# Kernel tuning notes

Measured on AMD Instinct MI355X. Metric: run time of the kernel, lower is better.

Reference implementation:

```python
import jax, jax.numpy as jnp
import numpy as np
from jax import lax

SINKHORN_ITERS = 20


def sinkhorn_knopp(logits, tau=1.0, iterations=SINKHORN_ITERS):
    # logits: [N, K]. Log-domain alternating row/col normalization.
    N, K = logits.shape
    P = logits / tau
    log_target_col_sum = jnp.log(jnp.asarray(N / K, dtype=logits.dtype) + 1e-9)

    def step(P, _):
        P = P - jax.nn.logsumexp(P, axis=1, keepdims=True)   # row sums -> 1
        P = P - jax.nn.logsumexp(P, axis=0, keepdims=True) + log_target_col_sum  # col sums -> N/K
        return P, None

    P, _ = lax.scan(step, P, None, length=iterations)
    return jnp.exp(P)


def setup_inputs() -> dict:
    key = jax.random.key(0)
    ks = jax.random.split(key, 8)
    N, C, K, B = 200000, 128, 32, 16
    x = jax.random.normal(ks[0], (N, C), dtype=jnp.float32)
    batch = jnp.sort(jax.random.randint(ks[1], (N,), 0, B))
    # assign_mlp: Linear(C,C) -> ReLU -> Linear(C,K)
    W1 = jax.random.normal(ks[2], (C, C), dtype=jnp.float32) / np.sqrt(C)
    b1 = jnp.zeros((C,), dtype=jnp.float32)
    W2 = jax.random.normal(ks[3], (C, K), dtype=jnp.float32) / np.sqrt(C)
    b2 = jnp.zeros((K,), dtype=jnp.float32)
    scaling = jnp.asarray(5.0, dtype=jnp.float32)
    return {"x": x, "batch": batch, "W1": W1, "b1": b1, "W2": W2, "b2": b2,
            "scaling": scaling, "num_graphs": B}


def reference(x, batch, W1, b1, W2, b2, scaling, num_graphs):
    # assignment logits: MLP(x) * scaling  -> [N, K]
    h = jax.nn.relu(x @ W1 + b1)
    logits = (h @ W2 + b2) * scaling
    # doubly-stochastic soft assignment via Sinkhorn-Knopp (tau=1.0, 20 iters)
    s = sinkhorn_knopp(logits, tau=1.0, iterations=SINKHORN_ITERS)  # [N, K]
    # pooled super-node features: scatter-sum over graphs of s[n,k]*x[n,c]
    onehot = jax.nn.one_hot(batch, num_graphs, dtype=x.dtype)        # [N, B]
    out = jnp.einsum('nb,nk,nc->bkc', onehot, s, x)                  # [B, K, C]
    return out
```

## Files before the change

### kernel.cpp

```cpp
#include <hip/hip_runtime.h>
#include <hip/hip_bf16.h>

#define C_DIM 128
#define K_DIM 32
#define N_ITERS 20
#define SPAD 132
#define NSHARD 8

__global__ void init_kernel(float* __restrict__ out, float* __restrict__ vcs,
                            int n_out, int n_vcs) {
    int i = blockIdx.x * blockDim.x + threadIdx.x;
    int stride = gridDim.x * blockDim.x;
    for (int j = i; j < n_out; j += stride) out[j] = 0.f;
    for (int j = i; j < n_vcs; j += stride) vcs[j] = 0.f;
}

__global__ __launch_bounds__(1024, 4) void mlp_kernel(
    const float* __restrict__ x, const float* __restrict__ W1,
    const float* __restrict__ b1, const float* __restrict__ W2,
    const float* __restrict__ b2, const float* __restrict__ scal,
    float* __restrict__ Lg, int N, int ntiles) {
    __shared__ float sW1[C_DIM * C_DIM];
    __shared__ float sW2[C_DIM * K_DIM];
    __shared__ float sB1[C_DIM];
    __shared__ float sB2[K_DIM];
    __shared__ float sT[128][SPAD];

    const int tid = threadIdx.x;
    for (int i = tid; i < C_DIM * C_DIM / 4; i += 1024)
        ((float4*)sW1)[i] = ((const float4*)W1)[i];
    for (int i = tid; i < C_DIM * K_DIM / 4; i += 1024)
        ((float4*)sW2)[i] = ((const float4*)W2)[i];
    if (tid < C_DIM / 4) ((float4*)sB1)[tid] = ((const float4*)b1)[tid];
    if (tid < K_DIM / 4) ((float4*)sB2)[tid] = ((const float4*)b2)[tid];
    const float sc = *scal;

    const int wave = tid >> 6;
    const int lane = tid & 63;
    const int r0 = wave * 8;

    for (int tile = blockIdx.x; tile < ntiles; tile += gridDim.x) {
        const int row0 = tile * 128;
        const int rows = min(128, N - row0);
        __syncthreads();
        {
            const float4* src = (const float4*)(x + (size_t)row0 * C_DIM);
            for (int i = tid; i < rows * 32; i += 1024) {
                const int r = i >> 5, cq = i & 31;
                ((float4*)&sT[r][0])[cq] = src[i];
            }
        }
        __syncthreads();

        float acc[8][2];
#pragma unroll
        for (int r = 0; r < 8; ++r) {
            acc[r][0] = sB1[2 * lane];
            acc[r][1] = sB1[2 * lane + 1];
        }
#pragma unroll 2
        for (int kc = 0; kc < 32; ++kc) {
            const int k = kc * 4;
            const float2 w0 = *(const float2*)&sW1[(k + 0) * C_DIM + 2 * lane];
            const float2 w1 = *(const float2*)&sW1[(k + 1) * C_DIM + 2 * lane];
            const float2 w2 = *(const float2*)&sW1[(k + 2) * C_DIM + 2 * lane];
            const float2 w3 = *(const float2*)&sW1[(k + 3) * C_DIM + 2 * lane];
#pragma unroll
            for (int r = 0; r < 8; ++r) {
                const float4 xv = *(const float4*)&sT[r0 + r][k];
                acc[r][0] = fmaf(xv.x, w0.x, acc[r][0]);
                acc[r][1] = fmaf(xv.x, w0.y, acc[r][1]);
                acc[r][0] = fmaf(xv.y, w1.x, acc[r][0]);
                acc[r][1] = fmaf(xv.y, w1.y, acc[r][1]);
                acc[r][0] = fmaf(xv.z, w2.x, acc[r][0]);
                acc[r][1] = fmaf(xv.z, w2.y, acc[r][1]);
                acc[r][0] = fmaf(xv.w, w3.x, acc[r][0]);
                acc[r][1] = fmaf(xv.w, w3.y, acc[r][1]);
            }
        }
#pragma unroll
        for (int r = 0; r < 8; ++r) {
            float2 hv;
            hv.x = fmaxf(acc[r][0], 0.f);
            hv.y = fmaxf(acc[r][1], 0.f);
            *(float2*)&sT[r0 + r][2 * lane] = hv;
        }

        const int r2 = lane & 7;
        const int kk0 = (lane >> 3) * 4;
        float a2[4];
        a2[0] = sB2[kk0];
        a2[1] = sB2[kk0 + 1];
        a2[2] = sB2[kk0 + 2];
        a2[3] = sB2[kk0 + 3];
#pragma unroll 4
        for (int c = 0; c < C_DIM; c += 4) {
            const float4 hv = *(const float4*)&sT[r0 + r2][c];
            const float4 q0 = *(const float4*)&sW2[(c + 0) * K_DIM + kk0];
            const float4 q1 = *(const float4*)&sW2[(c + 1) * K_DIM + kk0];
            const float4 q2 = *(const float4*)&sW2[(c + 2) * K_DIM + kk0];
            const float4 q3 = *(const float4*)&sW2[(c + 3) * K_DIM + kk0];
            a2[0] = fmaf(hv.x, q0.x, a2[0]); a2[1] = fmaf(hv.x, q0.y, a2[1]);
            a2[2] = fmaf(hv.x, q0.z, a2[2]); a2[3] = fmaf(hv.x, q0.w, a2[3]);
            a2[0] = fmaf(hv.y, q1.x, a2[0]); a2[1] = fmaf(hv.y, q1.y, a2[1]);
            a2[2] = fmaf(hv.y, q1.z, a2[2]); a2[3] = fmaf(hv.y, q1.w, a2[3]);
            a2[0] = fmaf(hv.z, q2.x, a2[0]); a2[1] = fmaf(hv.z, q2.y, a2[1]);
            a2[2] = fmaf(hv.z, q2.z, a2[2]); a2[3] = fmaf(hv.z, q2.w, a2[3]);
            a2[0] = fmaf(hv.w, q3.x, a2[0]); a2[1] = fmaf(hv.w, q3.y, a2[1]);
            a2[2] = fmaf(hv.w, q3.z, a2[2]); a2[3] = fmaf(hv.w, q3.w, a2[3]);
        }
        const int g = row0 + r0 + r2;
        if (g < N) {
            float4 o = make_float4(a2[0] * sc, a2[1] * sc, a2[2] * sc, a2[3] * sc);
            *(float4*)&Lg[(size_t)g * K_DIM + kk0] = o;
        }
    }
}

__device__ __forceinline__ int bitrev5(int l) {
    return ((l & 1) << 4) | ((l & 2) << 2) | (l & 4) | ((l & 8) >> 2) |
           ((l & 16) >> 4);
}

#define FOLD_STAGE(M, HALF)                                   \
    {                                                         \
        const bool hi = (lane & (M)) != 0;                    \
        _Pragma("unroll")                                     \
        for (int j = 0; j < (HALF); ++j) {                    \
            const float give = hi ? p[j] : p[j + (HALF)];     \
            const float keep = hi ? p[j + (HALF)] : p[j];     \
            p[j] = keep + __shfl_xor(give, (M));              \
        }                                                     \
    }

__global__ __launch_bounds__(1024) void sinkhorn_iter_kernel(
    const float* __restrict__ Lg, float* __restrict__ vbuf,
    float* __restrict__ shards, int t, int N) {
    __shared__ float sv[K_DIM];
    __shared__ float swsum[16][K_DIM];
    const int tid = threadIdx.x;
    const int wave = tid >> 6;
    const int lane = tid & 63;

    if (tid < K_DIM) {
        float vp = 0.f;
        if (t > 1) {
            float cs = 0.f;
#pragma unroll
            for (int sh = 0; sh < NSHARD; ++sh)
                cs += shards[((size_t)(t - 1) * NSHARD + sh) * K_DIM + tid];
            vp = vbuf[(t - 2) * K_DIM + tid] + __logf(cs) -
                 __logf((float)N / (float)K_DIM);
        }
        sv[tid] = vp;
        if (blockIdx.x == 0) vbuf[(t - 1) * K_DIM + tid] = vp;
    }
    __syncthreads();

    const size_t n = (size_t)blockIdx.x * 1024 + tid;
    float p[K_DIM];
    if (n < (size_t)N) {
        const float4* Lr = (const float4*)(Lg + n * K_DIM);
#pragma unroll
        for (int j = 0; j < 8; ++j) {
            const float4 lv = Lr[j];
            p[4 * j + 0] = lv.x - sv[4 * j + 0];
            p[4 * j + 1] = lv.y - sv[4 * j + 1];
            p[4 * j + 2] = lv.z - sv[4 * j + 2];
            p[4 * j + 3] = lv.w - sv[4 * j + 3];
        }
        float m0 = p[0];
#pragma unroll
        for (int j = 1; j < K_DIM; ++j) m0 = fmaxf(m0, p[j]);
        float sum = 0.f;
#pragma unroll
        for (int j = 0; j < K_DIM; ++j) {
            p[j] = __expf(p[j] - m0);
            sum += p[j];
        }
        const float inv = 1.f / sum;
#pragma unroll
        for (int j = 0; j < K_DIM; ++j) p[j] *= inv;
    } else {
#pragma unroll
        for (int j = 0; j < K_DIM; ++j) p[j] = 0.f;
    }

    FOLD_STAGE(1, 16)
    FOLD_STAGE(2, 8)
    FOLD_STAGE(4, 4)
    FOLD_STAGE(8, 2)
    FOLD_STAGE(16, 1)
    const float tot = p[0] + __shfl_xor(p[0], 32);
    if (lane < K_DIM) swsum[wave][bitrev5(lane)] = tot;
    __syncthreads();
    if (tid < K_DIM) {
        float s_ = 0.f;
#pragma unroll
        for (int w = 0; w < 16; ++w) s_ += swsum[w][tid];
        atomicAdd(&shards[((size_t)t * NSHARD + (blockIdx.x & (NSHARD - 1))) *
                              K_DIM + tid], s_);
    }
}

#define PCHUNK 96
#define PCH_PER_BLOCK 4

__global__ __launch_bounds__(256) void pool_kernel(
    const float* __restrict__ x, const int* __restrict__ batch,
    const float* __restrict__ Lg, const float* __restrict__ vbuf,
    const float* __restrict__ shards, float* __restrict__ out, int N) {
    __shared__ float sx[PCHUNK][C_DIM];
    __shared__ float ss[PCHUNK][K_DIM];
    __shared__ int sb[PCHUNK];
    __shared__ float sv19[K_DIM];
    __shared__ float sd[K_DIM];

    const int tid = threadIdx.x;
    if (tid < K_DIM) {
        sv19[tid] = vbuf[(N_ITERS - 1) * K_DIM + tid];
        float cs = 0.f;
#pragma unroll
        for (int sh = 0; sh < NSHARD; ++sh)
            cs += shards[((size_t)N_ITERS * NSHARD + sh) * K_DIM + tid];
        sd[tid] = ((float)N / (float)K_DIM) / cs;
    }
    __syncthreads();

    const int k0 = (tid >> 5) * 4;
    const int c0 = (tid & 31) * 4;
    float acc[4][4];
#pragma unroll
    for (int i = 0; i < 4; ++i)
#pragma unroll
        for (int j = 0; j < 4; ++j) acc[i][j] = 0.f;

    int cur_b = -1;
    const int base0 = blockIdx.x * (PCHUNK * PCH_PER_BLOCK);

    for (int cc = 0; cc < PCH_PER_BLOCK; ++cc) {
        const int base = base0 + cc * PCHUNK;
        if (base >= N) break;
        const int rows = min(PCHUNK, N - base);
        __syncthreads();
        {
            const float4* src = (const float4*)(x + (size_t)base * C_DIM);
            for (int i = tid; i < rows * (C_DIM / 4); i += 256)
                ((float4*)&sx[0][0])[i] = src[i];
        }
        if (tid < rows) {
            sb[tid] = batch[base + tid];
            const int n = base + tid;
            const float4* Lr = (const float4*)(Lg + (size_t)n * K_DIM);
            float p[K_DIM];
#pragma unroll
            for (int j = 0; j < 8; ++j) {
                const float4 lv = Lr[j];
                p[4 * j + 0] = lv.x - sv19[4 * j + 0];
                p[4 * j + 1] = lv.y - sv19[4 * j + 1];
                p[4 * j + 2] = lv.z - sv19[4 * j + 2];
                p[4 * j + 3] = lv.w - sv19[4 * j + 3];
            }
            float m0 = p[0];
#pragma unroll
            for (int j = 1; j < K_DIM; ++j) m0 = fmaxf(m0, p[j]);
            float sum = 0.f;
#pragma unroll
            for (int j = 0; j < K_DIM; ++j) {
                p[j] = __expf(p[j] - m0);
                sum += p[j];
            }
            const float inv = 1.f / sum;
#pragma unroll
            for (int j = 0; j < K_DIM; ++j) ss[tid][j] = p[j] * inv * sd[j];
        }
        __syncthreads();

        for (int r = 0; r < rows; ++r) {
            const int b = sb[r];
            if (b != cur_b) {
                if (cur_b >= 0) {
                    float* ob = out + ((size_t)cur_b * K_DIM + k0) * C_DIM + c0;
#pragma unroll
                    for (int i = 0; i < 4; ++i)
#pragma unroll
                        for (int j = 0; j < 4; ++j) {
                            atomicAdd(&ob[i * C_DIM + j], acc[i][j]);
                            acc[i][j] = 0.f;
                        }
                }
                cur_b = b;
            }
            const float4 sv = *(const float4*)&ss[r][k0];
            const float4 xv = *(const float4*)&sx[r][c0];
            const float sA[4] = {sv.x, sv.y, sv.z, sv.w};
            const float xA[4] = {xv.x, xv.y, xv.z, xv.w};
#pragma unroll
            for (int i = 0; i < 4; ++i)
#pragma unroll
                for (int j = 0; j < 4; ++j)
                    acc[i][j] = fmaf(sA[i], xA[j], acc[i][j]);
        }
    }
    if (cur_b >= 0) {
        float* ob = out + ((size_t)cur_b * K_DIM + k0) * C_DIM + c0;
#pragma unroll
        for (int i = 0; i < 4; ++i)
#pragma unroll
            for (int j = 0; j < 4; ++j) atomicAdd(&ob[i * C_DIM + j], acc[i][j]);
    }
}

extern "C" void kernel_launch(void* const* d_in, const int* in_sizes, int n_in,
                              void* d_out, int out_size, void* d_ws, size_t ws_size,
                              hipStream_t stream) {
    const float* x = (const float*)d_in[0];
    const int* batch = (const int*)d_in[1];
    const float* W1 = (const float*)d_in[2];
    const float* b1 = (const float*)d_in[3];
    const float* W2 = (const float*)d_in[4];
    const float* b2 = (const float*)d_in[5];
    const float* scal = (const float*)d_in[6];
    float* out = (float*)d_out;

    const int N = in_sizes[1];

    float* Lg = (float*)d_ws;
    float* vbuf = Lg + (size_t)N * K_DIM;
    float* shards = vbuf + (N_ITERS + 1) * K_DIM;
    const int n_vcs = (N_ITERS + 1) * K_DIM + (N_ITERS + 1) * NSHARD * K_DIM;

    init_kernel<<<64, 256, 0, stream>>>(out, vbuf, out_size, n_vcs);

    const int ntiles = (N + 127) / 128;
    mlp_kernel<<<256, 1024, 0, stream>>>(x, W1, b1, W2, b2, scal, Lg, N, ntiles);

    const int iblocks = (N + 1023) / 1024;
    for (int t = 1; t <= N_ITERS; ++t)
        sinkhorn_iter_kernel<<<iblocks, 1024, 0, stream>>>(Lg, vbuf, shards, t, N);

    const int pblocks = (N + PCHUNK * PCH_PER_BLOCK - 1) / (PCHUNK * PCH_PER_BLOCK);
    pool_kernel<<<pblocks, 256, 0, stream>>>(x, batch, Lg, vbuf, shards, out, N);
}
```

Baseline: 561.1 us.

## Use bf16 MFMA for MLP and fuse Sinkhorn iterations into persistent kernel

The MLP now converts x and the weights to bf16 and runs both layers on MFMA 16x16x32 instructions instead of scalar FP32 FMAs. The twenty per-iteration Sinkhorn launches are replaced by one kernel that keeps each row's logits in registers and uses a global arrival counter as a grid barrier between iterations. That kernel writes the final assignment matrix, so the pool kernel no longer recomputes the softmax. The grid barrier needs all 196 blocks of 1024 threads resident at once or it deadlocks, and bf16 inputs reduce logit precision.

New measurement: 1.422 ms. +153.5%, slower.

```diff
diff --git a/kernel.cpp b/kernel.cpp
--- a/kernel.cpp
+++ b/kernel.cpp
@@ -4,115 +4,117 @@
 #define C_DIM 128
 #define K_DIM 32
 #define N_ITERS 20
-#define SPAD 132
-#define NSHARD 8
-
-__global__ void init_kernel(float* __restrict__ out, float* __restrict__ vcs,
-                            int n_out, int n_vcs) {
+#define NSHARD 16
+#define WPAD 136
+
+typedef __attribute__((ext_vector_type(8))) short short8;
+typedef __attribute__((ext_vector_type(4))) float f32x4;
+typedef __attribute__((ext_vector_type(4))) unsigned short us4;
+
+__device__ __forceinline__ unsigned short f2bf(float f) {
+    __hip_bfloat16 h = __float2bfloat16(f);
+    return *reinterpret_cast<unsigned short*>(&h);
+}
+
+__global__ void init_kernel(float* __restrict__ out, int n_out,
+                            float* __restrict__ zreg, int n_z,
+                            const float* __restrict__ W1, const float* __restrict__ W2,
+                            unsigned short* __restrict__ W1t,
+                            unsigned short* __restrict__ W2t) {
     int i = blockIdx.x * blockDim.x + threadIdx.x;
     int stride = gridDim.x * blockDim.x;
     for (int j = i; j < n_out; j += stride) out[j] = 0.f;
-    for (int j = i; j < n_vcs; j += stride) vcs[j] = 0.f;
-}
-
-__global__ __launch_bounds__(1024, 4) void mlp_kernel(
-    const float* __restrict__ x, const float* __restrict__ W1,
-    const float* __restrict__ b1, const float* __restrict__ W2,
+    for (int j = i; j < n_z; j += stride) zreg[j] = 0.f;
+    for (int j = i; j < C_DIM * C_DIM; j += stride) {
+        int n = j >> 7, k = j & 127;
+        W1t[j] = f2bf(W1[k * C_DIM + n]);
+    }
+    for (int j = i; j < C_DIM * K_DIM; j += stride) {
+        int n = j >> 7, k = j & 127;
+        W2t[j] = f2bf(W2[k * K_DIM + n]);
+    }
+}
+
+__global__ __launch_bounds__(256, 4) void mlp_kernel(
+    const float* __restrict__ x, const unsigned short* __restrict__ W1t,
+    const float* __restrict__ b1, const unsigned short* __restrict__ W2t,
     const float* __restrict__ b2, const float* __restrict__ scal,
     float* __restrict__ Lg, int N, int ntiles) {
-    __shared__ float sW1[C_DIM * C_DIM];
-    __shared__ float sW2[C_DIM * K_DIM];
+    __shared__ unsigned short sW1[C_DIM][WPAD];
+    __shared__ unsigned short sW2[K_DIM][WPAD];
+    __shared__ unsigned short sX[64][WPAD];
+    __shared__ unsigned short sH[4][16][WPAD];
     __shared__ float sB1[C_DIM];
     __shared__ float sB2[K_DIM];
-    __shared__ float sT[128][SPAD];
 
     const int tid = threadIdx.x;
-    for (int i = tid; i < C_DIM * C_DIM / 4; i += 1024)
-        ((float4*)sW1)[i] = ((const float4*)W1)[i];
-    for (int i = tid; i < C_DIM * K_DIM / 4; i += 1024)
-        ((float4*)sW2)[i] = ((const float4*)W2)[i];
-    if (tid < C_DIM / 4) ((float4*)sB1)[tid] = ((const float4*)b1)[tid];
-    if (tid < K_DIM / 4) ((float4*)sB2)[tid] = ((const float4*)b2)[tid];
+    for (int i = tid; i < C_DIM * 16; i += 256) {
+        const int r = i >> 4, c8 = (i & 15) * 8;
+        *(float4*)&sW1[r][c8] = *(const float4*)&W1t[r * C_DIM + c8];
+    }
+    for (int i = tid; i < K_DIM * 16; i += 256) {
+        const int r = i >> 4, c8 = (i & 15) * 8;
+        *(float4*)&sW2[r][c8] = *(const float4*)&W2t[r * C_DIM + c8];
+    }
+    if (tid < C_DIM) sB1[tid] = b1[tid];
+    if (tid < K_DIM) sB2[tid] = b2[tid];
     const float sc = *scal;
 
     const int wave = tid >> 6;
     const int lane = tid & 63;
-    const int r0 = wave * 8;
+    const int lr = lane & 15;
+    const int kg = lane >> 4;
+    __syncthreads();
 
     for (int tile = blockIdx.x; tile < ntiles; tile += gridDim.x) {
-        const int row0 = tile * 128;
-        const int rows = min(128, N - row0);
-        __syncthreads();
-        {
-            const float4* src = (const float4*)(x + (size_t)row0 * C_DIM);
-            for (int i = tid; i < rows * 32; i += 1024) {
-                const int r = i >> 5, cq = i & 31;
-                ((float4*)&sT[r][0])[cq] = src[i];
-            }
-        }
-        __syncthreads();
-
-        float acc[8][2];
-#pragma unroll
-        for (int r = 0; r < 8; ++r) {
-            acc[r][0] = sB1[2 * lane];
-            acc[r][1] = sB1[2 * lane + 1];
-        }
-#pragma unroll 2
-        for (int kc = 0; kc < 32; ++kc) {
-            const int k = kc * 4;
-            const float2 w0 = *(const float2*)&sW1[(k + 0) * C_DIM + 2 * lane];
-            const float2 w1 = *(const float2*)&sW1[(k + 1) * C_DIM + 2 * lane];
-            const float2 w2 = *(const float2*)&sW1[(k + 2) * C_DIM + 2 * lane];
-            const float2 w3 = *(const float2*)&sW1[(k + 3) * C_DIM + 2 * lane];
-#pragma unroll
-            for (int r = 0; r < 8; ++r) {
-                const float4 xv = *(const float4*)&sT[r0 + r][k];
-                acc[r][0] = fmaf(xv.x, w0.x, acc[r][0]);
-                acc[r][1] = fmaf(xv.x, w0.y, acc[r][1]);
-                acc[r][0] = fmaf(xv.y, w1.x, acc[r][0]);
-                acc[r][1] = fmaf(xv.y, w1.y, acc[r][1]);
-                acc[r][0] = fmaf(xv.z, w2.x, acc[r][0]);
-                acc[r][1] = fmaf(xv.z, w2.y, acc[r][1]);
-                acc[r][0] = fmaf(xv.w, w3.x, acc[r][0]);
-                acc[r][1] = fmaf(xv.w, w3.y, acc[r][1]);
-            }
-        }
-#pragma unroll
-        for (int r = 0; r < 8; ++r) {
-            float2 hv;
-            hv.x = fmaxf(acc[r][0], 0.f);
-            hv.y = fmaxf(acc[r][1], 0.f);
-            *(float2*)&sT[r0 + r][2 * lane] = hv;
-        }
-
-        const int r2 = lane & 7;
-        const int kk0 = (lane >> 3) * 4;
-        float a2[4];
-        a2[0] = sB2[kk0];
-        a2[1] = sB2[kk0 + 1];
-        a2[2] = sB2[kk0 + 2];
-        a2[3] = sB2[kk0 + 3];
-#pragma unroll 4
-        for (int c = 0; c < C_DIM; c += 4) {
-            const float4 hv = *(const float4*)&sT[r0 + r2][c];
-            const float4 q0 = *(const float4*)&sW2[(c + 0) * K_DIM + kk0];
-            const float4 q1 = *(const float4*)&sW2[(c + 1) * K_DIM + kk0];
-            const float4 q2 = *(const float4*)&sW2[(c + 2) * K_DIM + kk0];
-            const float4 q3 = *(const float4*)&sW2[(c + 3) * K_DIM + kk0];
-            a2[0] = fmaf(hv.x, q0.x, a2[0]); a2[1] = fmaf(hv.x, q0.y, a2[1]);
-            a2[2] = fmaf(hv.x, q0.z, a2[2]); a2[3] = fmaf(hv.x, q0.w, a2[3]);
-            a2[0] = fmaf(hv.y, q1.x, a2[0]); a2[1] = fmaf(hv.y, q1.y, a2[1]);
-            a2[2] = fmaf(hv.y, q1.z, a2[2]); a2[3] = fmaf(hv.y, q1.w, a2[3]);
-            a2[0] = fmaf(hv.z, q2.x, a2[0]); a2[1] = fmaf(hv.z, q2.y, a2[1]);
-            a2[2] = fmaf(hv.z, q2.z, a2[2]); a2[3] = fmaf(hv.z, q2.w, a2[3]);
-            a2[0] = fmaf(hv.w, q3.x, a2[0]); a2[1] = fmaf(hv.w, q3.y, a2[1]);
-            a2[2] = fmaf(hv.w, q3.z, a2[2]); a2[3] = fmaf(hv.w, q3.w, a2[3]);
-        }
-        const int g = row0 + r0 + r2;
-        if (g < N) {
-            float4 o = make_float4(a2[0] * sc, a2[1] * sc, a2[2] * sc, a2[3] * sc);
-            *(float4*)&Lg[(size_t)g * K_DIM + kk0] = o;
+        const int row0 = tile * 64;
+        __syncthreads();
+        for (int i = tid; i < 2048; i += 256) {
+            const int r = i >> 5, c4 = (i & 31) * 4;
+            const float4 v = *(const float4*)&x[(size_t)(row0 + r) * C_DIM + c4];
+            us4 u;
+            u.x = f2bf(v.x); u.y = f2bf(v.y); u.z = f2bf(v.z); u.w = f2bf(v.w);
+            *(us4*)&sX[r][c4] = u;
+        }
+        __syncthreads();
+
+        short8 a[4];
+#pragma unroll
+        for (int kt = 0; kt < 4; ++kt)
+            a[kt] = *(const short8*)&sX[wave * 16 + lr][kt * 32 + kg * 8];
+#pragma unroll
+        for (int ct = 0; ct < 8; ++ct) {
+            const float bv = sB1[ct * 16 + lr];
+            f32x4 acc = {bv, bv, bv, bv};
+#pragma unroll
+            for (int kt = 0; kt < 4; ++kt) {
+                const short8 b = *(const short8*)&sW1[ct * 16 + lr][kt * 32 + kg * 8];
+                acc = __builtin_amdgcn_mfma_f32_16x16x32_bf16(a[kt], b, acc, 0, 0, 0);
+            }
+#pragma unroll
+            for (int r = 0; r < 4; ++r)
+                sH[wave][kg * 4 + r][ct * 16 + lr] = f2bf(fmaxf(acc[r], 0.f));
+        }
+        __syncthreads();
+
+        short8 a2[4];
+#pragma unroll
+        for (int kt = 0; kt < 4; ++kt)
+            a2[kt] = *(const short8*)&sH[wave][lr][kt * 32 + kg * 8];
+#pragma unroll
+        for (int ct = 0; ct < 2; ++ct) {
+            const float bv = sB2[ct * 16 + lr];
+            f32x4 acc = {bv, bv, bv, bv};
+#pragma unroll
+            for (int kt = 0; kt < 4; ++kt) {
+                const short8 b = *(const short8*)&sW2[ct * 16 + lr][kt * 32 + kg * 8];
+                acc = __builtin_amdgcn_mfma_f32_16x16x32_bf16(a2[kt], b, acc, 0, 0, 0);
+            }
+#pragma unroll
+            for (int r = 0; r < 4; ++r) {
+                const int g = row0 + wave * 16 + kg * 4 + r;
+                Lg[(size_t)g * K_DIM + ct * 16 + lr] = acc[r] * sc;
+            }
         }
     }
 }
@@ -133,73 +135,110 @@
         }                                                     \
     }
 
-__global__ __launch_bounds__(1024) void sinkhorn_iter_kernel(
-    const float* __restrict__ Lg, float* __restrict__ vbuf,
-    float* __restrict__ shards, int t, int N) {
+__global__ __launch_bounds__(1024, 4) void sinkhorn_kernel(
+    float* __restrict__ Lg, float* __restrict__ shards, int* __restrict__ arrive,
+    int N, int nblocks) {
     __shared__ float sv[K_DIM];
     __shared__ float swsum[16][K_DIM];
+    __shared__ float sdl[K_DIM];
     const int tid = threadIdx.x;
     const int wave = tid >> 6;
     const int lane = tid & 63;
-
-    if (tid < K_DIM) {
-        float vp = 0.f;
-        if (t > 1) {
+    const size_t n = (size_t)blockIdx.x * 1024 + tid;
+    const bool valid = n < (size_t)N;
+    const int myshard = blockIdx.x & (NSHARD - 1);
+    const float log_tgt = __logf((float)N / (float)K_DIM);
+
+    if (tid < K_DIM) sv[tid] = 0.f;
+
+    float L[K_DIM];
+    if (valid) {
+        const float4* Lr = (const float4*)(Lg + n * K_DIM);
+#pragma unroll
+        for (int j = 0; j < 8; ++j) {
+            const float4 v = Lr[j];
+            L[4 * j] = v.x; L[4 * j + 1] = v.y; L[4 * j + 2] = v.z; L[4 * j + 3] = v.w;
+        }
+    } else {
+#pragma unroll
+        for (int j = 0; j < K_DIM; ++j) L[j] = 0.f;
+    }
+    __syncthreads();
+
+    float m0 = 0.f, inv = 0.f;
+    for (int t = 1; t <= N_ITERS; ++t) {
+        float p[K_DIM];
+        if (valid) {
+#pragma unroll
+            for (int j = 0; j < K_DIM; ++j) p[j] = L[j] - sv[j];
+            m0 = p[0];
+#pragma unroll
+            for (int j = 1; j < K_DIM; ++j) m0 = fmaxf(m0, p[j]);
+            float sum = 0.f;
+#pragma unroll
+            for (int j = 0; j < K_DIM; ++j) {
+                p[j] = __expf(p[j] - m0);
+                sum += p[j];
+            }
+            inv = 1.f / sum;
+#pragma unroll
+            for (int j = 0; j < K_DIM; ++j) p[j] *= inv;
+        } else {
+#pragma unroll
+            for (int j = 0; j < K_DIM; ++j) p[j] = 0.f;
+        }
+
+        FOLD_STAGE(1, 16)
+        FOLD_STAGE(2, 8)
+        FOLD_STAGE(4, 4)
+        FOLD_STAGE(8, 2)
+        FOLD_STAGE(16, 1)
+        const float tot = p[0] + __shfl_xor(p[0], 32);
+        if (lane < K_DIM) swsum[wave][bitrev5(lane)] = tot;
+        __syncthreads();
+        if (tid < K_DIM) {
+            float s_ = 0.f;
+#pragma unroll
+            for (int w = 0; w < 16; ++w) s_ += swsum[w][tid];
+            atomicAdd(&shards[((size_t)t * NSHARD + myshard) * K_DIM + tid], s_);
+        }
+        __syncthreads();
+        __threadfence();
+        if (tid == 0) {
+            __hip_atomic_fetch_add(arrive + t, 1, __ATOMIC_RELEASE,
+                                   __HIP_MEMORY_SCOPE_AGENT);
+            while (__hip_atomic_load(arrive + t, __ATOMIC_ACQUIRE,
+                                     __HIP_MEMORY_SCOPE_AGENT) < nblocks)
+                __builtin_amdgcn_s_sleep(2);
+        }
+        __syncthreads();
+
+        if (tid < K_DIM) {
             float cs = 0.f;
 #pragma unroll
             for (int sh = 0; sh < NSHARD; ++sh)
-                cs += shards[((size_t)(t - 1) * NSHARD + sh) * K_DIM + tid];
-            vp = vbuf[(t - 2) * K_DIM + tid] + __logf(cs) -
-                 __logf((float)N / (float)K_DIM);
-        }
-        sv[tid] = vp;
-        if (blockIdx.x == 0) vbuf[(t - 1) * K_DIM + tid] = vp;
-    }
-    __syncthreads();
-
-    const size_t n = (size_t)blockIdx.x * 1024 + tid;
-    float p[K_DIM];
-    if (n < (size_t)N) {
-        const float4* Lr = (const float4*)(Lg + n * K_DIM);
+                cs += __hip_atomic_load(
+                    &shards[((size_t)t * NSHARD + sh) * K_DIM + tid],
+                    __ATOMIC_RELAXED, __HIP_MEMORY_SCOPE_AGENT);
+            if (t < N_ITERS)
+                sv[tid] += __logf(cs) - log_tgt;
+            else
+                sdl[tid] = ((float)N / (float)K_DIM) / cs;
+        }
+        __syncthreads();
+    }
+
+    if (valid) {
+        float4* Sr = (float4*)(Lg + n * K_DIM);
 #pragma unroll
         for (int j = 0; j < 8; ++j) {
-            const float4 lv = Lr[j];
-            p[4 * j + 0] = lv.x - sv[4 * j + 0];
-            p[4 * j + 1] = lv.y - sv[4 * j + 1];
-            p[4 * j + 2] = lv.z - sv[4 * j + 2];
-            p[4 * j + 3] = lv.w - sv[4 * j + 3];
-        }
-        float m0 = p[0];
-#pragma unroll
-        for (int j = 1; j < K_DIM; ++j) m0 = fmaxf(m0, p[j]);
-        float sum = 0.f;
-#pragma unroll
-        for (int j = 0; j < K_DIM; ++j) {
-            p[j] = __expf(p[j] - m0);
-            sum += p[j];
-        }
-        const float inv = 1.f / sum;
-#pragma unroll
-        for (int j = 0; j < K_DIM; ++j) p[j] *= inv;
-    } else {
-#pragma unroll
-        for (int j = 0; j < K_DIM; ++j) p[j] = 0.f;
-    }
-
-    FOLD_STAGE(1, 16)
-    FOLD_STAGE(2, 8)
-    FOLD_STAGE(4, 4)
-    FOLD_STAGE(8, 2)
-    FOLD_STAGE(16, 1)
-    const float tot = p[0] + __shfl_xor(p[0], 32);
-    if (lane < K_DIM) swsum[wave][bitrev5(lane)] = tot;
-    __syncthreads();
-    if (tid < K_DIM) {
-        float s_ = 0.f;
-#pragma unroll
-        for (int w = 0; w < 16; ++w) s_ += swsum[w][tid];
-        atomicAdd(&shards[((size_t)t * NSHARD + (blockIdx.x & (NSHARD - 1))) *
-                              K_DIM + tid], s_);
+            float4 o;
+            o.x = __expf(L[4 * j + 0] - sv[4 * j + 0] - m0) * inv * sdl[4 * j + 0];
+            o.y = __expf(L[4 * j + 1] - sv[4 * j + 1] - m0) * inv * sdl[4 * j + 1];
+            o.z = __expf(L[4 * j + 2] - sv[4 * j + 2] - m0) * inv * sdl[4 * j + 2];
+            o.w = __expf(L[4 * j + 3] - sv[4 * j + 3] - m0) * inv * sdl[4 * j + 3];
+            Sr[j] = o;
+        }
     }
 }
 
@@ -208,25 +247,12 @@
 
 __global__ __launch_bounds__(256) void pool_kernel(
     const float* __restrict__ x, const int* __restrict__ batch,
-    const float* __restrict__ Lg, const float* __restrict__ vbuf,
-    const float* __restrict__ shards, float* __restrict__ out, int N) {
+    const float* __restrict__ Sg, float* __restrict__ out, int N) {
     __shared__ float sx[PCHUNK][C_DIM];
     __shared__ float ss[PCHUNK][K_DIM];
     __shared__ int sb[PCHUNK];
-    __shared__ float sv19[K_DIM];
-    __shared__ float sd[K_DIM];
 
     const int tid = threadIdx.x;
-    if (tid < K_DIM) {
-        sv19[tid] = vbuf[(N_ITERS - 1) * K_DIM + tid];
-        float cs = 0.f;
-#pragma unroll
-        for (int sh = 0; sh < NSHARD; ++sh)
-            cs += shards[((size_t)N_ITERS * NSHARD + sh) * K_DIM + tid];
-        sd[tid] = ((float)N / (float)K_DIM) / cs;
-    }
-    __syncthreads();
-
     const int k0 = (tid >> 5) * 4;
     const int c0 = (tid & 31) * 4;
     float acc[4][4];
@@ -247,33 +273,11 @@
             const float4* src = (const float4*)(x + (size_t)base * C_DIM);
             for (int i = tid; i < rows * (C_DIM / 4); i += 256)
                 ((float4*)&sx[0][0])[i] = src[i];
-        }
-        if (tid < rows) {
-            sb[tid] = batch[base + tid];
-            const int n = base + tid;
-            const float4* Lr = (const float4*)(Lg + (size_t)n * K_DIM);
-            float p[K_DIM];
-#pragma unroll
-            for (int j = 0; j < 8; ++j) {
-                const float4 lv = Lr[j];
-                p[4 * j + 0] = lv.x - sv19[4 * j + 0];
-                p[4 * j + 1] = lv.y - sv19[4 * j + 1];
-                p[4 * j + 2] = lv.z - sv19[4 * j + 2];
-                p[4 * j + 3] = lv.w - sv19[4 * j + 3];
-            }
-            float m0 = p[0];
-#pragma unroll
-            for (int j = 1; j < K_DIM; ++j) m0 = fmaxf(m0, p[j]);
-            float sum = 0.f;
-#pragma unroll
-            for (int j = 0; j < K_DIM; ++j) {
-                p[j] = __expf(p[j] - m0);
-                sum += p[j];
-            }
-            const float inv = 1.f / sum;
-#pragma unroll
-            for (int j = 0; j < K_DIM; ++j) ss[tid][j] = p[j] * inv * sd[j];
-        }
+            const float4* ssrc = (const float4*)(Sg + (size_t)base * K_DIM);
+            for (int i = tid; i < rows * (K_DIM / 4); i += 256)
+                ((float4*)&ss[0][0])[i] = ssrc[i];
+        }
+        if (tid < rows) sb[tid] = batch[base + tid];
         __syncthreads();
 
         for (int r = 0; r < rows; ++r) {
@@ -326,19 +330,21 @@
     const int N = in_sizes[1];
 
     float* Lg = (float*)d_ws;
-    float* vbuf = Lg + (size_t)N * K_DIM;
-    float* shards = vbuf + (N_ITERS + 1) * K_DIM;
-    const int n_vcs = (N_ITERS + 1) * K_DIM + (N_ITERS + 1) * NSHARD * K_DIM;
-
-    init_kernel<<<64, 256, 0, stream>>>(out, vbuf, out_size, n_vcs);
-
-    const int ntiles = (N + 127) / 128;
-    mlp_kernel<<<256, 1024, 0, stream>>>(x, W1, b1, W2, b2, scal, Lg, N, ntiles);
-
-    const int iblocks = (N + 1023) / 1024;
-    for (int t = 1; t <= N_ITERS; ++t)
-        sinkhorn_iter_kernel<<<iblocks, 1024, 0, stream>>>(Lg, vbuf, shards, t, N);
+    float* shards = Lg + (size_t)N * K_DIM;
+    const int n_shard_f = (N_ITERS + 1) * NSHARD * K_DIM;
+    int* arrive = (int*)(shards + n_shard_f);
+    unsigned short* W1t = (unsigned short*)(arrive + 64);
+    unsigned short* W2t = W1t + C_DIM * C_DIM;
+
+    init_kernel<<<64, 256, 0, stream>>>(out, out_size, shards, n_shard_f + 64,
+                                        W1, W2, W1t, W2t);
+
+    const int ntiles = N / 64;
+    mlp_kernel<<<640, 256, 0, stream>>>(x, W1t, b1, W2t, b2, scal, Lg, N, ntiles);
+
+    const int sblocks = (N + 1023) / 1024;
+    sinkhorn_kernel<<<sblocks, 1024, 0, stream>>>(Lg, shards, arrive, N, sblocks);
 
     const int pblocks = (N + PCHUNK * PCH_PER_BLOCK - 1) / (PCHUNK * PCH_PER_BLOCK);
-    pool_kernel<<<pblocks, 256, 0, stream>>>(x, batch, Lg, vbuf, shards, out, N);
-}
+    pool_kernel<<<pblocks, 256, 0, stream>>>(x, batch, Lg, out, N);
+}
```
